# Performance work log

Measured on AMD Instinct MI355X. Metric: run time of the kernel, lower is better.

## Reference

```python
import jax, jax.numpy as jnp
import numpy as np

DIM = 96
D_STATE = 16
D_CONV = 3
D_INNER = 192   # int(DIM * 2.0)
DT_RANK = 6     # ceil(DIM / 16)
K = 4           # cross-scan directions
BATCH, H, W = 2, 56, 56


def setup_inputs() -> dict:
    key = jax.random.key(0)
    k = jax.random.split(key, 8)
    x = jax.random.normal(k[0], (BATCH, DIM, H, W), jnp.float32)
    W_in = jax.random.normal(k[1], (DIM, 2 * D_INNER), jnp.float32) / np.sqrt(DIM)
    W_conv = jax.random.normal(k[2], (D_INNER, 1, D_CONV, D_CONV), jnp.float32) / D_CONV
    b_conv = jnp.zeros((D_INNER,), jnp.float32)
    W_xproj = jax.random.normal(k[3], (K, D_INNER, DT_RANK + 2 * D_STATE), jnp.float32) / np.sqrt(D_INNER)
    W_dt = jax.random.normal(k[4], (K, DT_RANK, D_INNER), jnp.float32) / np.sqrt(DT_RANK)
    # dt bias init as in torch: dt ~ exp(U * (log 0.1 - log 0.001) + log 0.001), inv-softplus
    dt = jnp.exp(jax.random.uniform(k[5], (K, D_INNER), jnp.float32)
                 * (np.log(0.1) - np.log(0.001)) + np.log(0.001))
    dt = jnp.clip(dt, 1e-4, None)
    b_dt = dt + jnp.log(-jnp.expm1(-dt))
    A_logs = jnp.log(jnp.broadcast_to(jnp.arange(1, D_STATE + 1, dtype=jnp.float32),
                                      (K, D_INNER, D_STATE)))
    Ds = jnp.ones((K, D_INNER), jnp.float32)
    W_out = jax.random.normal(k[6], (D_INNER, DIM), jnp.float32) / np.sqrt(D_INNER)
    return dict(x=x, W_in=W_in, W_conv=W_conv, b_conv=b_conv, W_xproj=W_xproj,
                W_dt=W_dt, b_dt=b_dt, A_logs=A_logs, Ds=Ds, W_out=W_out)


def _ss2d(x, W_in, W_conv, b_conv, W_xproj, W_dt, b_dt, A_logs, Ds, W_out):
    Bsz, C, Hh, Ww = x.shape
    L = Hh * Ww
    # in_proj
    xf = x.transpose(0, 2, 3, 1).reshape(Bsz, L, C)        # (B, L, C)
    xz = xf @ W_in
    xp, z = jnp.split(xz, 2, axis=-1)                       # each (B, L, D)
    # depthwise conv + silu
    xi = xp.reshape(Bsz, Hh, Ww, -1).transpose(0, 3, 1, 2)  # (B, D, H, W)
    pad = D_CONV // 2
    xi = jax.lax.conv_general_dilated(
        xi, W_conv, (1, 1), ((pad, pad), (pad, pad)),
        feature_group_count=xi.shape[1],
        dimension_numbers=('NCHW', 'OIHW', 'NCHW')) + b_conv[None, :, None, None]
    xi = jax.nn.silu(xi)
    D = xi.shape[1]
    # cross-scan: 4 directions, each (B, L, D)
    x1 = xi.reshape(Bsz, D, L).transpose(0, 2, 1)
    x2 = xi[:, :, :, ::-1].reshape(Bsz, D, L).transpose(0, 2, 1)
    xt = xi.transpose(0, 1, 3, 2)                           # (B, D, W, H)
    x3 = xt.reshape(Bsz, D, L).transpose(0, 2, 1)
    x4 = xt[:, :, :, ::-1].reshape(Bsz, D, L).transpose(0, 2, 1)
    xs = jnp.stack([x1, x2, x3, x4])                        # (K, B, L, D)
    # per-direction projections, batched over K
    xdbl = jnp.einsum('kbld,kde->kble', xs, W_xproj)
    dr = xdbl[..., :DT_RANK]
    Bk = xdbl[..., DT_RANK:DT_RANK + D_STATE]               # (K, B, L, N)
    Ck = xdbl[..., DT_RANK + D_STATE:]                      # (K, B, L, N)
    delta = jax.nn.softplus(jnp.einsum('kblr,krd->kbld', dr, W_dt)
                            + b_dt[:, None, None, :])       # (K, B, L, D)
    A = -jnp.exp(A_logs)                                    # (K, D, N)

    def step(h, inp):
        x_i, d_i, B_i, C_i = inp  # (K,B,D), (K,B,D), (K,B,N), (K,B,N)
        dA = jnp.exp(d_i[..., None] * A[:, None])           # (K, B, D, N)
        h = dA * h + (d_i * x_i)[..., None] * B_i[:, :, None, :]
        y = jnp.einsum('kbdn,kbn->kbd', h, C_i)
        return h, y

    h0 = jnp.zeros((K, Bsz, D, D_STATE), xs.dtype)
    seq = (xs.transpose(2, 0, 1, 3), delta.transpose(2, 0, 1, 3),
           Bk.transpose(2, 0, 1, 3), Ck.transpose(2, 0, 1, 3))
    _, ys = jax.lax.scan(step, h0, seq)                     # (L, K, B, D)
    ys = ys.transpose(1, 2, 0, 3) + xs * Ds[:, None, None, :]  # (K, B, L, D)
    # cross-merge back to row-major (h w) order
    y1 = ys[0]
    y2 = ys[1].reshape(Bsz, Hh, Ww, D)[:, :, ::-1, :].reshape(Bsz, L, D)
    y3 = ys[2].reshape(Bsz, Ww, Hh, D).transpose(0, 2, 1, 3).reshape(Bsz, L, D)
    y4 = ys[3].reshape(Bsz, Ww, Hh, D)[:, :, ::-1, :].transpose(0, 2, 1, 3).reshape(Bsz, L, D)
    y = (y1 + y2 + y3 + y4) * jax.nn.silu(z)
    out = (y @ W_out).reshape(Bsz, Hh, Ww, C).transpose(0, 3, 1, 2)
    return out


def reference(x, W_in, W_conv, b_conv, W_xproj, W_dt, b_dt, A_logs, Ds, W_out):
    return _ss2d(x, W_in, W_conv, b_conv, W_xproj, W_dt, b_dt, A_logs, Ds, W_out)
```

## Files before the change

### kernel.cpp

```cpp
#include <hip/hip_runtime.h>
#include <math.h>

constexpr int BATCH  = 2;
constexpr int CDIM   = 96;
constexpr int HH     = 56;
constexpr int WW     = 56;
constexpr int LL     = HH * WW;
constexpr int DIN    = 192;
constexpr int NK     = 4;
constexpr int NST    = 16;
constexpr int RNK    = 6;
constexpr int EPROJ  = RNK + 2 * NST;
constexpr int SCH    = 64;
constexpr int NCH    = LL / SCH;
constexpr int CGRP   = DIN / 16;

constexpr size_t SZ_PX   = (size_t)BATCH * LL * DIN;
constexpr size_t OFF_XP  = 0;
constexpr size_t OFF_Z   = OFF_XP + SZ_PX;
constexpr size_t OFF_XI  = OFF_Z  + SZ_PX;
constexpr size_t OFF_DR  = OFF_XI + SZ_PX;
constexpr size_t SZ_DR   = (size_t)NK * BATCH * LL * 8;
constexpr size_t OFF_B   = OFF_DR + SZ_DR;
constexpr size_t SZ_BC   = (size_t)NK * BATCH * LL * NST;
constexpr size_t OFF_C   = OFF_B + SZ_BC;
constexpr size_t OFF_Y   = OFF_C + SZ_BC;
constexpr size_t SZ_HS   = (size_t)NK * BATCH * NCH * DIN * NST;
constexpr size_t OFF_HE  = OFF_Y + SZ_PX;
constexpr size_t OFF_HI  = OFF_HE + SZ_HS;
constexpr size_t OFF_WT  = OFF_HI + SZ_HS;
constexpr size_t SZ_WT   = (size_t)NK * EPROJ * DIN;

__device__ __forceinline__ float silu(float v) {
    return v / (1.0f + __expf(-v));
}

__device__ __forceinline__ float softplus_f(float x) {
    return (x > 20.0f) ? x : __logf(1.0f + __expf(x));
}

__device__ __forceinline__ float row_reduce16(float p) {
    p += __int_as_float(__builtin_amdgcn_update_dpp(0, __float_as_int(p), 0x128, 0xf, 0xf, true));
    p += __int_as_float(__builtin_amdgcn_update_dpp(0, __float_as_int(p), 0x124, 0xf, 0xf, true));
    p += __int_as_float(__builtin_amdgcn_update_dpp(0, __float_as_int(p), 0x122, 0xf, 0xf, true));
    p += __int_as_float(__builtin_amdgcn_update_dpp(0, __float_as_int(p), 0x121, 0xf, 0xf, true));
    return p;
}

__device__ __forceinline__ int seq_to_lr(int k, int l) {
    int q = l / WW;
    int r = l - q * WW;
    if (k == 0) return l;
    if (k == 1) return q * WW + (WW - 1 - r);
    if (k == 2) return r * WW + q;
    return (WW - 1 - r) * WW + q;
}

__device__ __forceinline__ int spatial_to_seq(int k, int s) {
    int h = s / WW;
    int w = s - h * WW;
    if (k == 0) return s;
    if (k == 1) return h * WW + (WW - 1 - w);
    if (k == 2) return w * WW + h;
    return w * WW + (WW - 1 - h);
}

__device__ __forceinline__ size_t hs_idx(int c, int kb, int d, int n) {
    return ((size_t)(c * (NK * BATCH) + kb) * DIN + d) * NST + n;
}

__global__ __launch_bounds__(256) void k_wt(
        const float* __restrict__ W_xproj, float* __restrict__ Wt) {
    int i = blockIdx.x * 256 + threadIdx.x;
    if (i >= NK * DIN * EPROJ) return;
    int k = i / (DIN * EPROJ);
    int r = i % (DIN * EPROJ);
    int d = r / EPROJ;
    int e = r % EPROJ;
    Wt[((size_t)k * EPROJ + e) * DIN + d] = W_xproj[i];
}

constexpr int K1_PIX = 8;
__global__ __launch_bounds__(384) void k_inproj(
        const float* __restrict__ x, const float* __restrict__ W_in,
        float* __restrict__ xp, float* __restrict__ z) {
    __shared__ float sxT[CDIM][K1_PIX];
    int gp0 = blockIdx.x * K1_PIX;
    int t   = threadIdx.x;
    int b   = gp0 / LL;
    int l0  = gp0 - b * LL;
    for (int i = t; i < CDIM * K1_PIX; i += 384) {
        int c = i >> 3, p = i & 7;
        sxT[c][p] = x[((size_t)(b * CDIM + c)) * LL + l0 + p];
    }
    __syncthreads();
    int e = t;
    float acc[K1_PIX];
#pragma unroll
    for (int p = 0; p < K1_PIX; p++) acc[p] = 0.0f;
    const float4* sx4 = (const float4*)sxT;
#pragma unroll 4
    for (int c = 0; c < CDIM; c++) {
        float w  = W_in[c * (2 * DIN) + e];
        float4 va = sx4[2 * c];
        float4 vb = sx4[2 * c + 1];
        acc[0] = fmaf(va.x, w, acc[0]); acc[1] = fmaf(va.y, w, acc[1]);
        acc[2] = fmaf(va.z, w, acc[2]); acc[3] = fmaf(va.w, w, acc[3]);
        acc[4] = fmaf(vb.x, w, acc[4]); acc[5] = fmaf(vb.y, w, acc[5]);
        acc[6] = fmaf(vb.z, w, acc[6]); acc[7] = fmaf(vb.w, w, acc[7]);
    }
    if (e < DIN) {
#pragma unroll
        for (int p = 0; p < K1_PIX; p++)
            xp[((size_t)(gp0 + p)) * DIN + e] = acc[p];
    } else {
        int e2 = e - DIN;
#pragma unroll
        for (int p = 0; p < K1_PIX; p++)
            z[((size_t)(gp0 + p)) * DIN + e2] = acc[p];
    }
}

__global__ __launch_bounds__(192) void k_conv(
        const float* __restrict__ xp, const float* __restrict__ Wc,
        const float* __restrict__ bc, float* __restrict__ xi) {
    int gp = blockIdx.x;
    int d  = threadIdx.x;
    int b  = gp / LL;
    int l  = gp - b * LL;
    int h  = l / WW;
    int w  = l - h * WW;
    float acc = bc[d];
#pragma unroll
    for (int dy = -1; dy <= 1; dy++) {
        int hh = h + dy;
        if (hh < 0 || hh >= HH) continue;
#pragma unroll
        for (int dx = -1; dx <= 1; dx++) {
            int ww = w + dx;
            if (ww < 0 || ww >= WW) continue;
            acc = fmaf(xp[((size_t)b * LL + hh * WW + ww) * DIN + d],
                       Wc[d * 9 + (dy + 1) * 3 + (dx + 1)], acc);
        }
    }
    xi[(size_t)gp * DIN + d] = silu(acc);
}

constexpr int K3_PIX = 32;
__global__ __launch_bounds__(256) void k_xproj(
        const float* __restrict__ xi, const float* __restrict__ Wt,
        const float* __restrict__ Ds,
        float* __restrict__ drbuf, float* __restrict__ Bbuf,
        float* __restrict__ Cbuf, float* __restrict__ ysum) {
    __shared__ float4 v4[K3_PIX][49];
    __shared__ float4 sw4[EPROJ][49];
    int k   = blockIdx.y;
    int gp0 = blockIdx.x * K3_PIX;
    int b   = gp0 / LL;
    int l0  = gp0 - b * LL;
    int t   = threadIdx.x;
    const float4* xin4 = (const float4*)(xi + (size_t)gp0 * DIN);
    for (int i = t; i < K3_PIX * 48; i += 256)
        v4[i / 48][i % 48] = xin4[i];
    const float4* wt4 = (const float4*)(Wt + (size_t)k * EPROJ * DIN);
    for (int i = t; i < EPROJ * 48; i += 256)
        sw4[i / 48][i % 48] = wt4[i];
    __syncthreads();
    if (k == 0) {
        const float* vf = (const float*)v4;
        for (int i = t; i < K3_PIX * DIN; i += 256) {
            int p = i / DIN, d = i % DIN;
            float dsum = Ds[d] + Ds[DIN + d] + Ds[2 * DIN + d] + Ds[3 * DIN + d];
            ysum[(size_t)gp0 * DIN + i] = vf[p * 196 + d] * dsum;
        }
    }
    int p0 = t & 15;
    int eg = t >> 4;
    bool has3 = (eg < EPROJ - 32);
    float acc[2][3] = {{0.f, 0.f, 0.f}, {0.f, 0.f, 0.f}};
    for (int j = 0; j < 48; j++) {
        float4 w0 = sw4[eg][j];
        float4 w1 = sw4[eg + 16][j];
        float4 w2 = has3 ? sw4[eg + 32][j] : make_float4(0.f, 0.f, 0.f, 0.f);
#pragma unroll
        for (int q = 0; q < 2; q++) {
            float4 vv = v4[p0 + 16 * q][j];
            acc[q][0] = fmaf(vv.x, w0.x, acc[q][0]); acc[q][0] = fmaf(vv.y, w0.y, acc[q][0]);
            acc[q][0] = fmaf(vv.z, w0.z, acc[q][0]); acc[q][0] = fmaf(vv.w, w0.w, acc[q][0]);
            acc[q][1] = fmaf(vv.x, w1.x, acc[q][1]); acc[q][1] = fmaf(vv.y, w1.y, acc[q][1]);
            acc[q][1] = fmaf(vv.z, w1.z, acc[q][1]); acc[q][1] = fmaf(vv.w, w1.w, acc[q][1]);
            acc[q][2] = fmaf(vv.x, w2.x, acc[q][2]); acc[q][2] = fmaf(vv.y, w2.y, acc[q][2]);
            acc[q][2] = fmaf(vv.z, w2.z, acc[q][2]); acc[q][2] = fmaf(vv.w, w2.w, acc[q][2]);
        }
    }
#pragma unroll
    for (int q = 0; q < 2; q++) {
        int p  = p0 + 16 * q;
        int ls = spatial_to_seq(k, l0 + p);
        size_t kb  = (size_t)(k * BATCH + b);
        size_t b8  = (kb * LL + ls) * 8;
        size_t b16 = (kb * LL + ls) * NST;
        if (eg < RNK) drbuf[b8 + eg] = acc[q][0];
        else          Bbuf[b16 + eg - RNK] = acc[q][0];
        int e1 = eg + 16;
        if (e1 < RNK + NST) Bbuf[b16 + e1 - RNK] = acc[q][1];
        else                Cbuf[b16 + e1 - RNK - NST] = acc[q][1];
        if (has3) Cbuf[b16 + eg + 32 - RNK - NST] = acc[q][2];
    }
}

__global__ __launch_bounds__(256) void k_scanA(
        const float* __restrict__ xi, const float* __restrict__ drbuf,
        const float* __restrict__ Bbuf, const float* __restrict__ A_logs,
        const float* __restrict__ W_dt, const float* __restrict__ b_dt,
        float* __restrict__ Pbuf, float* __restrict__ hend) {
    __shared__ float2 sDU2[16][SCH + 2];
    __shared__ float  sB1t[16][SCH + 4];
    int c   = blockIdx.x;
    int blk = blockIdx.y;
    int k   = blk / (BATCH * CGRP);
    int rem = blk % (BATCH * CGRP);
    int b   = rem / CGRP;
    int cg  = rem % CGRP;
    int d0  = cg * 16;
    int t    = threadIdx.x;
    int lane = t & 63, wave = t >> 6;
    int grp  = lane >> 4, n = lane & 15;
    int ch   = wave * 4 + grp;
    int d    = d0 + ch;
    float A = -__expf(A_logs[((size_t)(k * DIN + d)) * NST + n]);
    size_t kb = (size_t)(k * BATCH + b);
    const float* drp = drbuf + kb * LL * 8;
    const float* bp  = Bbuf  + kb * LL * NST;
    const float* up  = xi    + (size_t)b * LL * DIN;
    int dloc = d0 + (t & 15);
    float bb = b_dt[k * DIN + dloc];
    float w0 = W_dt[((size_t)k * RNK + 0) * DIN + dloc];
    float w1 = W_dt[((size_t)k * RNK + 1) * DIN + dloc];
    float w2 = W_dt[((size_t)k * RNK + 2) * DIN + dloc];
    float w3 = W_dt[((size_t)k * RNK + 3) * DIN + dloc];
    float w4 = W_dt[((size_t)k * RNK + 4) * DIN + dloc];
    float w5 = W_dt[((size_t)k * RNK + 5) * DIN + dloc];
    int l0 = c * SCH;
    for (int i = t; i < SCH * 16; i += 256) {
        int s = i >> 4, cc = i & 15;
        int l = l0 + s;
        int lr = seq_to_lr(k, l);
        float4 r03 = *(const float4*)(drp + (size_t)l * 8);
        float2 r45 = *(const float2*)(drp + (size_t)l * 8 + 4);
        float raw = bb;
        raw = fmaf(r03.x, w0, raw); raw = fmaf(r03.y, w1, raw);
        raw = fmaf(r03.z, w2, raw); raw = fmaf(r03.w, w3, raw);
        raw = fmaf(r45.x, w4, raw); raw = fmaf(r45.y, w5, raw);
        float dlt = softplus_f(raw);
        float u = up[(size_t)lr * DIN + d0 + cc];
        sDU2[cc][s] = make_float2(dlt, dlt * u);
        sB1t[cc][s] = bp[(size_t)l * NST + cc];
    }
    __syncthreads();
    float h = 0.0f, P = 1.0f;
#pragma unroll 2
    for (int s4 = 0; s4 < SCH; s4 += 4) {
        float4 duA = *(const float4*)&sDU2[ch][s4];
        float4 duB = *(const float4*)&sDU2[ch][s4 + 2];
        float4 bq  = *(const float4*)&sB1t[n][s4];
        float dA;
        dA = __expf(duA.x * A); h = fmaf(dA, h, duA.y * bq.x); P *= dA;
        dA = __expf(duA.z * A); h = fmaf(dA, h, duA.w * bq.y); P *= dA;
        dA = __expf(duB.x * A); h = fmaf(dA, h, duB.y * bq.z); P *= dA;
        dA = __expf(duB.z * A); h = fmaf(dA, h, duB.w * bq.w); P *= dA;
    }
    size_t idx = hs_idx(c, (int)kb, d, n);
    Pbuf[idx] = P;
    hend[idx] = h;
}

__global__ __launch_bounds__(256) void k_scanB(
        const float* __restrict__ Pbuf, const float* __restrict__ hend,
        float* __restrict__ hin) {
    int tid = blockIdx.x * 256 + threadIdx.x;
    int kb  = tid / (DIN * NST);
    int dn  = tid % (DIN * NST);
    float h = 0.0f;
    for (int c = 0; c < NCH; c++) {
        size_t idx = ((size_t)(c * (NK * BATCH) + kb)) * (DIN * NST) + dn;
        hin[idx] = h;
        h = fmaf(Pbuf[idx], h, hend[idx]);
    }
}

__global__ __launch_bounds__(256) void k_scanC(
        const float* __restrict__ xi, const float* __restrict__ drbuf,
        const float* __restrict__ Bbuf, const float* __restrict__ Cbuf,
        const float* __restrict__ A_logs, const float* __restrict__ W_dt,
        const float* __restrict__ b_dt, const float* __restrict__ hin,
        float* __restrict__ ysum) {
    __shared__ float2 sDU2[16][SCH + 2];
    __shared__ float2 sBC2[16][SCH + 2];
    __shared__ float  sY[16][SCH + 4];
    int c   = blockIdx.x;
    int blk = blockIdx.y;
    int k   = blk / (BATCH * CGRP);
    int rem = blk % (BATCH * CGRP);
    int b   = rem / CGRP;
    int cg  = rem % CGRP;
    int d0  = cg * 16;
    int t    = threadIdx.x;
    int lane = t & 63, wave = t >> 6;
    int grp  = lane >> 4, n = lane & 15;
    int ch   = wave * 4 + grp;
    int d    = d0 + ch;
    float A = -__expf(A_logs[((size_t)(k * DIN + d)) * NST + n]);
    size_t kb = (size_t)(k * BATCH + b);
    const float* drp = drbuf + kb * LL * 8;
    const float* bp  = Bbuf  + kb * LL * NST;
    const float* cp  = Cbuf  + kb * LL * NST;
    const float* up  = xi    + (size_t)b * LL * DIN;
    float*       yp  = ysum  + (size_t)b * LL * DIN;
    int dloc = d0 + (t & 15);
    float bb = b_dt[k * DIN + dloc];
    float w0 = W_dt[((size_t)k * RNK + 0) * DIN + dloc];
    float w1 = W_dt[((size_t)k * RNK + 1) * DIN + dloc];
    float w2 = W_dt[((size_t)k * RNK + 2) * DIN + dloc];
    float w3 = W_dt[((size_t)k * RNK + 3) * DIN + dloc];
    float w4 = W_dt[((size_t)k * RNK + 4) * DIN + dloc];
    float w5 = W_dt[((size_t)k * RNK + 5) * DIN + dloc];
    int l0 = c * SCH;
    for (int i = t; i < SCH * 16; i += 256) {
        int s = i >> 4, cc = i & 15;
        int l = l0 + s;
        int lr = seq_to_lr(k, l);
        float4 r03 = *(const float4*)(drp + (size_t)l * 8);
        float2 r45 = *(const float2*)(drp + (size_t)l * 8 + 4);
        float raw = bb;
        raw = fmaf(r03.x, w0, raw); raw = fmaf(r03.y, w1, raw);
        raw = fmaf(r03.z, w2, raw); raw = fmaf(r03.w, w3, raw);
        raw = fmaf(r45.x, w4, raw); raw = fmaf(r45.y, w5, raw);
        float dlt = softplus_f(raw);
        float u = up[(size_t)lr * DIN + d0 + cc];
        sDU2[cc][s] = make_float2(dlt, dlt * u);
        sBC2[cc][s] = make_float2(bp[(size_t)l * NST + cc],
                                  cp[(size_t)l * NST + cc]);
    }
    float h = hin[hs_idx(c, (int)kb, d, n)];
    __syncthreads();
#pragma unroll 2
    for (int s4 = 0; s4 < SCH; s4 += 4) {
        float4 duA = *(const float4*)&sDU2[ch][s4];
        float4 duB = *(const float4*)&sDU2[ch][s4 + 2];
        float4 bcA = *(const float4*)&sBC2[n][s4];
        float4 bcB = *(const float4*)&sBC2[n][s4 + 2];
        float dA, y0, y1, y2, y3;
        dA = __expf(duA.x * A); h = fmaf(dA, h, duA.y * bcA.x); y0 = row_reduce16(h * bcA.y);
        dA = __expf(duA.z * A); h = fmaf(dA, h, duA.w * bcA.z); y1 = row_reduce16(h * bcA.w);
        dA = __expf(duB.x * A); h = fmaf(dA, h, duB.y * bcB.x); y2 = row_reduce16(h * bcB.y);
        dA = __expf(duB.z * A); h = fmaf(dA, h, duB.w * bcB.z); y3 = row_reduce16(h * bcB.w);
        if (n == 0) *(float4*)&sY[ch][s4] = make_float4(y0, y1, y2, y3);
    }
    __syncthreads();
    for (int i = t; i < SCH * 16; i += 256) {
        int s = i >> 4, cc = i & 15;
        int lr = seq_to_lr(k, l0 + s);
        atomicAdd(&yp[(size_t)lr * DIN + d0 + cc], sY[cc][s]);
    }
}

constexpr int K5_PIX = 8;
__global__ __launch_bounds__(192) void k_out(
        const float* __restrict__ ysum, const float* __restrict__ zbuf,
        const float* __restrict__ W_out, float* __restrict__ out) {
    __shared__ float g[DIN][12];
    __shared__ float so[CDIM][9];
    int gp0 = blockIdx.x * K5_PIX;
    int b   = gp0 / LL;
    int l0  = gp0 - b * LL;
    int t   = threadIdx.x;
    for (int i = t; i < K5_PIX * DIN; i += 192) {
        int p = i / DIN, dd = i % DIN;
        size_t idx = (size_t)(gp0 + p) * DIN + dd;
        g[dd][p] = ysum[idx] * silu(zbuf[idx]);
    }
    __syncthreads();
    int f    = t % CDIM;
    int half = t / CDIM;
    float acc[4] = {0.f, 0.f, 0.f, 0.f};
#pragma unroll 4
    for (int dd = 0; dd < DIN; dd++) {
        float wv = W_out[dd * CDIM + f];
        float4 gv = *(const float4*)&g[dd][half * 4];
        acc[0] = fmaf(gv.x, wv, acc[0]);
        acc[1] = fmaf(gv.y, wv, acc[1]);
        acc[2] = fmaf(gv.z, wv, acc[2]);
        acc[3] = fmaf(gv.w, wv, acc[3]);
    }
#pragma unroll
    for (int p = 0; p < 4; p++) so[f][half * 4 + p] = acc[p];
    __syncthreads();
    for (int i = t; i < CDIM * K5_PIX; i += 192) {
        int f2 = i / K5_PIX, p2 = i % K5_PIX;
        out[((size_t)(b * CDIM + f2)) * LL + l0 + p2] = so[f2][p2];
    }
}

extern "C" void kernel_launch(void* const* d_in, const int* in_sizes, int n_in,
                              void* d_out, int out_size, void* d_ws, size_t ws_size,
                              hipStream_t stream) {
    const float* x       = (const float*)d_in[0];
    const float* W_in    = (const float*)d_in[1];
    const float* W_conv  = (const float*)d_in[2];
    const float* b_conv  = (const float*)d_in[3];
    const float* W_xproj = (const float*)d_in[4];
    const float* W_dt    = (const float*)d_in[5];
    const float* b_dt    = (const float*)d_in[6];
    const float* A_logs  = (const float*)d_in[7];
    const float* Ds      = (const float*)d_in[8];
    const float* W_out   = (const float*)d_in[9];
    float* out = (float*)d_out;
    float* ws  = (float*)d_ws;

    float* xp    = ws + OFF_XP;
    float* z     = ws + OFF_Z;
    float* xi    = ws + OFF_XI;
    float* drbuf = ws + OFF_DR;
    float* Bbuf  = ws + OFF_B;
    float* Cbuf  = ws + OFF_C;
    float* ysum  = ws + OFF_Y;
    float* hend  = ws + OFF_HE;
    float* hin   = ws + OFF_HI;
    float* Wt    = ws + OFF_WT;
    float* Pbuf  = xp;

    k_wt<<<(NK * DIN * EPROJ + 255) / 256, 256, 0, stream>>>(W_xproj, Wt);
    k_inproj<<<(BATCH * LL) / K1_PIX, 384, 0, stream>>>(x, W_in, xp, z);
    k_conv<<<BATCH * LL, DIN, 0, stream>>>(xp, W_conv, b_conv, xi);
    dim3 g3((BATCH * LL) / K3_PIX, NK);
    k_xproj<<<g3, 256, 0, stream>>>(xi, Wt, Ds, drbuf, Bbuf, Cbuf, ysum);
    dim3 gs(NCH, NK * BATCH * CGRP);
    k_scanA<<<gs, 256, 0, stream>>>(xi, drbuf, Bbuf, A_logs, W_dt, b_dt, Pbuf, hend);
    k_scanB<<<(NK * BATCH * DIN * NST) / 256, 256, 0, stream>>>(Pbuf, hend, hin);
    k_scanC<<<gs, 256, 0, stream>>>(xi, drbuf, Bbuf, Cbuf, A_logs, W_dt, b_dt, hin, ysum);
    k_out<<<(BATCH * LL) / K5_PIX, 192, 0, stream>>>(ysum, z, W_out, out);
}
```

Before: 209.5 us.

## Replace scan atomics with per-direction output buffers summed in out-projection

The scan's final stage now writes each direction's output to its own buffer with plain stores instead of atomically adding into one shared sum. The out-projection kernel sums the four direction buffers and adds the D skip term itself, so the xproj kernel no longer initialises the sum. The weight-transpose kernel is folded into the in-projection kernel to remove one launch. This removes atomic contention but writes and reads four times as much intermediate y data.

```diff
diff --git a/kernel.cpp b/kernel.cpp
--- a/kernel.cpp
+++ b/kernel.cpp
@@ -24,9 +24,10 @@
 constexpr size_t OFF_B   = OFF_DR + SZ_DR;
 constexpr size_t SZ_BC   = (size_t)NK * BATCH * LL * NST;
 constexpr size_t OFF_C   = OFF_B + SZ_BC;
-constexpr size_t OFF_Y   = OFF_C + SZ_BC;
+constexpr size_t OFF_YD  = OFF_C + SZ_BC;
+constexpr size_t SZ_YD   = (size_t)NK * BATCH * LL * DIN;
+constexpr size_t OFF_HE  = OFF_YD + SZ_YD;
 constexpr size_t SZ_HS   = (size_t)NK * BATCH * NCH * DIN * NST;
-constexpr size_t OFF_HE  = OFF_Y + SZ_PX;
 constexpr size_t OFF_HI  = OFF_HE + SZ_HS;
 constexpr size_t OFF_WT  = OFF_HI + SZ_HS;
 constexpr size_t SZ_WT   = (size_t)NK * EPROJ * DIN;
@@ -69,26 +70,24 @@
     return ((size_t)(c * (NK * BATCH) + kb) * DIN + d) * NST + n;
 }
 
-__global__ __launch_bounds__(256) void k_wt(
-        const float* __restrict__ W_xproj, float* __restrict__ Wt) {
-    int i = blockIdx.x * 256 + threadIdx.x;
-    if (i >= NK * DIN * EPROJ) return;
-    int k = i / (DIN * EPROJ);
-    int r = i % (DIN * EPROJ);
-    int d = r / EPROJ;
-    int e = r % EPROJ;
-    Wt[((size_t)k * EPROJ + e) * DIN + d] = W_xproj[i];
-}
-
 constexpr int K1_PIX = 8;
 __global__ __launch_bounds__(384) void k_inproj(
         const float* __restrict__ x, const float* __restrict__ W_in,
-        float* __restrict__ xp, float* __restrict__ z) {
+        const float* __restrict__ W_xproj,
+        float* __restrict__ xp, float* __restrict__ z, float* __restrict__ Wt) {
     __shared__ float sxT[CDIM][K1_PIX];
     int gp0 = blockIdx.x * K1_PIX;
     int t   = threadIdx.x;
     int b   = gp0 / LL;
     int l0  = gp0 - b * LL;
+    int gid = blockIdx.x * 384 + t;
+    if (gid < NK * DIN * EPROJ) {
+        int k = gid / (DIN * EPROJ);
+        int r = gid % (DIN * EPROJ);
+        int d = r / EPROJ;
+        int e = r % EPROJ;
+        Wt[((size_t)k * EPROJ + e) * DIN + d] = W_xproj[gid];
+    }
     for (int i = t; i < CDIM * K1_PIX; i += 384) {
         int c = i >> 3, p = i & 7;
         sxT[c][p] = x[((size_t)(b * CDIM + c)) * LL + l0 + p];
@@ -149,9 +148,8 @@
 constexpr int K3_PIX = 32;
 __global__ __launch_bounds__(256) void k_xproj(
         const float* __restrict__ xi, const float* __restrict__ Wt,
-        const float* __restrict__ Ds,
         float* __restrict__ drbuf, float* __restrict__ Bbuf,
-        float* __restrict__ Cbuf, float* __restrict__ ysum) {
+        float* __restrict__ Cbuf) {
     __shared__ float4 v4[K3_PIX][49];
     __shared__ float4 sw4[EPROJ][49];
     int k   = blockIdx.y;
@@ -166,14 +164,6 @@
     for (int i = t; i < EPROJ * 48; i += 256)
         sw4[i / 48][i % 48] = wt4[i];
     __syncthreads();
-    if (k == 0) {
-        const float* vf = (const float*)v4;
-        for (int i = t; i < K3_PIX * DIN; i += 256) {
-            int p = i / DIN, d = i % DIN;
-            float dsum = Ds[d] + Ds[DIN + d] + Ds[2 * DIN + d] + Ds[3 * DIN + d];
-            ysum[(size_t)gp0 * DIN + i] = vf[p * 196 + d] * dsum;
-        }
-    }
     int p0 = t & 15;
     int eg = t >> 4;
     bool has3 = (eg < EPROJ - 32);
@@ -294,7 +284,7 @@
         const float* __restrict__ Bbuf, const float* __restrict__ Cbuf,
         const float* __restrict__ A_logs, const float* __restrict__ W_dt,
         const float* __restrict__ b_dt, const float* __restrict__ hin,
-        float* __restrict__ ysum) {
+        float* __restrict__ ydir) {
     __shared__ float2 sDU2[16][SCH + 2];
     __shared__ float2 sBC2[16][SCH + 2];
     __shared__ float  sY[16][SCH + 4];
@@ -316,7 +306,7 @@
     const float* bp  = Bbuf  + kb * LL * NST;
     const float* cp  = Cbuf  + kb * LL * NST;
     const float* up  = xi    + (size_t)b * LL * DIN;
-    float*       yp  = ysum  + (size_t)b * LL * DIN;
+    float*       yp  = ydir  + kb * LL * DIN;
     int dloc = d0 + (t & 15);
     float bb = b_dt[k * DIN + dloc];
     float w0 = W_dt[((size_t)k * RNK + 0) * DIN + dloc];
@@ -361,13 +351,14 @@
     for (int i = t; i < SCH * 16; i += 256) {
         int s = i >> 4, cc = i & 15;
         int lr = seq_to_lr(k, l0 + s);
-        atomicAdd(&yp[(size_t)lr * DIN + d0 + cc], sY[cc][s]);
+        yp[(size_t)lr * DIN + d0 + cc] = sY[cc][s];
     }
 }
 
 constexpr int K5_PIX = 8;
 __global__ __launch_bounds__(192) void k_out(
-        const float* __restrict__ ysum, const float* __restrict__ zbuf,
+        const float* __restrict__ ydir, const float* __restrict__ xi,
+        const float* __restrict__ zbuf, const float* __restrict__ Ds,
         const float* __restrict__ W_out, float* __restrict__ out) {
     __shared__ float g[DIN][12];
     __shared__ float so[CDIM][9];
@@ -377,8 +368,12 @@
     int t   = threadIdx.x;
     for (int i = t; i < K5_PIX * DIN; i += 192) {
         int p = i / DIN, dd = i % DIN;
-        size_t idx = (size_t)(gp0 + p) * DIN + dd;
-        g[dd][p] = ysum[idx] * silu(zbuf[idx]);
+        size_t off = (size_t)(gp0 + p) * DIN + dd;
+        float y = ydir[off] + ydir[SZ_PX + off]
+                + ydir[2 * SZ_PX + off] + ydir[3 * SZ_PX + off];
+        float dsum = Ds[dd] + Ds[DIN + dd] + Ds[2 * DIN + dd] + Ds[3 * DIN + dd];
+        y = fmaf(xi[off], dsum, y);
+        g[dd][p] = y * silu(zbuf[off]);
     }
     __syncthreads();
     int f    = t % CDIM;
@@ -424,20 +419,19 @@
     float* drbuf = ws + OFF_DR;
     float* Bbuf  = ws + OFF_B;
     float* Cbuf  = ws + OFF_C;
-    float* ysum  = ws + OFF_Y;
+    float* ydir  = ws + OFF_YD;
     float* hend  = ws + OFF_HE;
     float* hin   = ws + OFF_HI;
     float* Wt    = ws + OFF_WT;
     float* Pbuf  = xp;
 
-    k_wt<<<(NK * DIN * EPROJ + 255) / 256, 256, 0, stream>>>(W_xproj, Wt);
-    k_inproj<<<(BATCH * LL) / K1_PIX, 384, 0, stream>>>(x, W_in, xp, z);
+    k_inproj<<<(BATCH * LL) / K1_PIX, 384, 0, stream>>>(x, W_in, W_xproj, xp, z, Wt);
     k_conv<<<BATCH * LL, DIN, 0, stream>>>(xp, W_conv, b_conv, xi);
     dim3 g3((BATCH * LL) / K3_PIX, NK);
-    k_xproj<<<g3, 256, 0, stream>>>(xi, Wt, Ds, drbuf, Bbuf, Cbuf, ysum);
+    k_xproj<<<g3, 256, 0, stream>>>(xi, Wt, drbuf, Bbuf, Cbuf);
     dim3 gs(NCH, NK * BATCH * CGRP);
     k_scanA<<<gs, 256, 0, stream>>>(xi, drbuf, Bbuf, A_logs, W_dt, b_dt, Pbuf, hend);
     k_scanB<<<(NK * BATCH * DIN * NST) / 256, 256, 0, stream>>>(Pbuf, hend, hin);
-    k_scanC<<<gs, 256, 0, stream>>>(xi, drbuf, Bbuf, Cbuf, A_logs, W_dt, b_dt, hin, ysum);
-    k_out<<<(BATCH * LL) / K5_PIX, 192, 0, stream>>>(ysum, z, W_out, out);
-}
+    k_scanC<<<gs, 256, 0, stream>>>(xi, drbuf, Bbuf, Cbuf, A_logs, W_dt, b_dt, hin, ydir);
+    k_out<<<(BATCH * LL) / K5_PIX, 192, 0, stream>>>(ydir, xi, z, Ds, W_out, out);
+}
```

Result: no change. 208.6 us (-0.4%).
